# Kernel tuning notes

Hardware: AMD Instinct MI355X
Metric: run time of the kernel (lower is better)

The kernel has to match this reference:

```python
import jax, jax.numpy as jnp
import numpy as np

N = 100000       # nodes
E = 3200000      # edges (avg degree 32)
IN = 64          # in_channels
HID = 32         # hidden_channels
HEADS = 2
OUT = 1
EPS = 1e-5       # LayerNorm eps
SLOPE = 0.2      # LeakyReLU negative slope (PyG default)


def setup_inputs() -> dict:
    key = jax.random.key(0)
    ks = jax.random.split(key, 18)
    def nrm(k, shape, scale=0.1):
        return jax.random.normal(k, shape, dtype=jnp.float32) * scale
    return {
        "x": jax.random.normal(ks[0], (N, IN), dtype=jnp.float32),
        "edge_index": jax.random.randint(ks[1], (2, E), 0, N, dtype=jnp.int64),
        # GATConv layer 1 (concat=True)
        "W1": nrm(ks[2], (IN, HEADS * HID)),
        "a_src1": nrm(ks[3], (HEADS, HID)),
        "a_dst1": nrm(ks[4], (HEADS, HID)),
        "b1": jnp.zeros((HEADS * HID,), jnp.float32),
        "ln1_g": jnp.ones((HEADS * HID,), jnp.float32),
        "ln1_b": jnp.zeros((HEADS * HID,), jnp.float32),
        # GATConv layer 2 (heads=1, concat=False)
        "W2": nrm(ks[5], (HEADS * HID, HID)),
        "a_src2": nrm(ks[6], (1, HID)),
        "a_dst2": nrm(ks[7], (1, HID)),
        "b2": jnp.zeros((HID,), jnp.float32),
        "ln2_g": jnp.ones((HID,), jnp.float32),
        "ln2_b": jnp.zeros((HID,), jnp.float32),
        # output Linear
        "Wout": nrm(ks[8], (HID, OUT)),
        "bout": jnp.zeros((OUT,), jnp.float32),
    }


def layer_norm(x, g, b):
    mu = jnp.mean(x, axis=-1, keepdims=True)
    var = jnp.mean(jnp.square(x - mu), axis=-1, keepdims=True)
    return (x - mu) * jax.lax.rsqrt(var + EPS) * g + b


def gat_conv(x, edge_index, W, a_src, a_dst, bias, heads, ch, concat):
    """PyG GATConv (add_self_loops=True, bias=True), eval mode (no dropout)."""
    n = x.shape[0]
    loop = jnp.arange(n, dtype=edge_index.dtype)
    src = jnp.concatenate([edge_index[0], loop])   # [E+N]
    dst = jnp.concatenate([edge_index[1], loop])   # [E+N]
    h = (x @ W).reshape(n, heads, ch)              # [N,H,C]
    al_src = jnp.sum(h * a_src, axis=-1)           # [N,H]
    al_dst = jnp.sum(h * a_dst, axis=-1)           # [N,H]
    logits = jax.nn.leaky_relu(al_src[src] + al_dst[dst], SLOPE)  # [E+N,H]
    # segment softmax over destination nodes
    m = jax.lax.stop_gradient(jax.ops.segment_max(logits, dst, num_segments=n))
    e = jnp.exp(logits - m[dst])
    denom = jax.ops.segment_sum(e, dst, num_segments=n)
    alpha = e / denom[dst]                         # [E+N,H]
    out = jax.ops.segment_sum(h[src] * alpha[:, :, None], dst, num_segments=n)  # [N,H,C]
    out = out.reshape(n, heads * ch) if concat else out.mean(axis=1)
    return out + bias


def reference(x, edge_index, W1, a_src1, a_dst1, b1, ln1_g, ln1_b,
              W2, a_src2, a_dst2, b2, ln2_g, ln2_b, Wout, bout):
    h = gat_conv(x, edge_index, W1, a_src1, a_dst1, b1, HEADS, HID, True)
    h = jax.nn.elu(layer_norm(h, ln1_g, ln1_b))
    h = gat_conv(h, edge_index, W2, a_src2, a_dst2, b2, 1, HID, False)
    h = jax.nn.elu(layer_norm(h, ln2_g, ln2_b))
    return h @ Wout + bout  # [N, OUT]
```

## Files before the change

### kernel.cpp

```cpp
#include <hip/hip_runtime.h>

#define EPS 1e-5f
#define SLOPE 0.2f
#define MAXK 512
#define SEGCAP 12288
#define PBATCH 8192
#define AG1_SLOTS 8

__device__ __forceinline__ float leaky(float z) {
    return fmaxf(z, 0.f) + SLOPE * fminf(z, 0.f);
}
__device__ __forceinline__ ushort f2bf(float f) {
    unsigned u = __float_as_uint(f);
    u += 0x7FFFu + ((u >> 16) & 1u);
    return (ushort)(u >> 16);
}
__device__ __forceinline__ float bf2f(ushort b) {
    return __uint_as_float(((unsigned)b) << 16);
}
__device__ __forceinline__ float blo(unsigned u) {
    return __uint_as_float(u << 16);
}
__device__ __forceinline__ float bhi(unsigned u) {
    return __uint_as_float(u & 0xffff0000u);
}
__device__ __forceinline__ void gather16_to_lds(const void* g, void* l) {
    __builtin_amdgcn_global_load_lds(
        (const __attribute__((address_space(1))) void*)g,
        (__attribute__((address_space(3))) void*)l, 16, 0, 0);
}

__global__ __launch_bounds__(1024) void fused1(
    const int* __restrict__ ei, int E, int K, int* __restrict__ segcnt,
    unsigned* __restrict__ part,
    const float* __restrict__ x, const float* __restrict__ W1,
    const float* __restrict__ as1, const float* __restrict__ ad1,
    ushort* __restrict__ h1b, float* __restrict__ al_s, float* __restrict__ al_d,
    int N, int EB) {
    __shared__ float smem[4096 + 64 * 68];
    int t = threadIdx.x;
    if ((int)blockIdx.x < EB) {
        int* h   = (int*)smem;
        int* gp  = h + 512;
        int* run = h + 1024;
        for (int i = t; i < K; i += 1024) { h[i] = 0; run[i] = 0; }
        __syncthreads();
        int base = blockIdx.x * PBATCH;
        int sv[PBATCH / 1024], dv[PBATCH / 1024];
#pragma unroll
        for (int j = 0; j < PBATCH / 1024; j++) {
            int e = base + j * 1024 + t;
            sv[j] = (e < E) ? ei[e] : -1;
            dv[j] = (e < E) ? ei[E + e] : -1;
            if (dv[j] >= 0) atomicAdd(&h[dv[j] >> 8], 1);
        }
        __syncthreads();
        for (int i = t; i < K; i += 1024)
            gp[i] = h[i] ? atomicAdd(&segcnt[i * 16], h[i]) : 0;
        __syncthreads();
#pragma unroll
        for (int j = 0; j < PBATCH / 1024; j++) {
            if (dv[j] >= 0) {
                int b = dv[j] >> 8;
                int p = atomicAdd(&run[b], 1) + gp[b];
                if (p < SEGCAP)
                    part[(size_t)b * SEGCAP + p] =
                        ((unsigned)sv[j] << 8) | (unsigned)(dv[j] & 255);
            }
        }
        return;
    }
    float* Ws = smem;
    float (*xs)[68] = (float(*)[68])(smem + 4096);
    for (int i = t; i < 4096; i += 1024) Ws[i] = W1[i];
    int base = (blockIdx.x - EB) * 64;
    {
        int rr = t >> 4, kk = t & 15;
        int gr = base + rr;
        float4 vx = (gr < N) ? ((const float4*)x)[(size_t)gr * 16 + kk]
                             : make_float4(0.f, 0.f, 0.f, 0.f);
        *(float4*)&xs[rr][kk * 4] = vx;
    }
    __syncthreads();
    int wv = t >> 6, c = t & 63;
    int r0 = base + wv * 4;
    float acc0 = 0.f, acc1 = 0.f, acc2 = 0.f, acc3 = 0.f;
#pragma unroll
    for (int k = 0; k < 64; k += 4) {
        float4 x0 = *(const float4*)&xs[wv * 4 + 0][k];
        float4 x1 = *(const float4*)&xs[wv * 4 + 1][k];
        float4 x2 = *(const float4*)&xs[wv * 4 + 2][k];
        float4 x3 = *(const float4*)&xs[wv * 4 + 3][k];
        float w0 = Ws[(k + 0) * 64 + c];
        float w1 = Ws[(k + 1) * 64 + c];
        float w2 = Ws[(k + 2) * 64 + c];
        float w3 = Ws[(k + 3) * 64 + c];
        acc0 = fmaf(x0.x, w0, acc0); acc1 = fmaf(x1.x, w0, acc1);
        acc2 = fmaf(x2.x, w0, acc2); acc3 = fmaf(x3.x, w0, acc3);
        acc0 = fmaf(x0.y, w1, acc0); acc1 = fmaf(x1.y, w1, acc1);
        acc2 = fmaf(x2.y, w1, acc2); acc3 = fmaf(x3.y, w1, acc3);
        acc0 = fmaf(x0.z, w2, acc0); acc1 = fmaf(x1.z, w2, acc1);
        acc2 = fmaf(x2.z, w2, acc2); acc3 = fmaf(x3.z, w2, acc3);
        acc0 = fmaf(x0.w, w3, acc0); acc1 = fmaf(x1.w, w3, acc1);
        acc2 = fmaf(x2.w, w3, acc2); acc3 = fmaf(x3.w, w3, acc3);
    }
    int head = c >> 5, cc = c & 31;
    float asc = as1[head * 32 + cc], adc = ad1[head * 32 + cc];
    float vs0 = acc0 * asc, vd0 = acc0 * adc;
    float vs1 = acc1 * asc, vd1 = acc1 * adc;
    float vs2 = acc2 * asc, vd2 = acc2 * adc;
    float vs3 = acc3 * asc, vd3 = acc3 * adc;
#pragma unroll
    for (int off = 1; off < 32; off <<= 1) {
        vs0 += __shfl_xor(vs0, off); vd0 += __shfl_xor(vd0, off);
        vs1 += __shfl_xor(vs1, off); vd1 += __shfl_xor(vd1, off);
        vs2 += __shfl_xor(vs2, off); vd2 += __shfl_xor(vd2, off);
        vs3 += __shfl_xor(vs3, off); vd3 += __shfl_xor(vd3, off);
    }
    if (r0 + 0 < N) h1b[(size_t)(r0 + 0) * 64 + c] = f2bf(acc0);
    if (r0 + 1 < N) h1b[(size_t)(r0 + 1) * 64 + c] = f2bf(acc1);
    if (r0 + 2 < N) h1b[(size_t)(r0 + 2) * 64 + c] = f2bf(acc2);
    if (r0 + 3 < N) h1b[(size_t)(r0 + 3) * 64 + c] = f2bf(acc3);
    if (cc == 0) {
        if (r0 + 0 < N) { al_s[(r0 + 0) * 2 + head] = vs0; al_d[(r0 + 0) * 2 + head] = vd0; }
        if (r0 + 1 < N) { al_s[(r0 + 1) * 2 + head] = vs1; al_d[(r0 + 1) * 2 + head] = vd1; }
        if (r0 + 2 < N) { al_s[(r0 + 2) * 2 + head] = vs2; al_d[(r0 + 2) * 2 + head] = vd2; }
        if (r0 + 3 < N) { al_s[(r0 + 3) * 2 + head] = vs3; al_d[(r0 + 3) * 2 + head] = vd3; }
    }
}

__global__ __launch_bounds__(1024) void sortseg(
    const int* __restrict__ segcnt, int N,
    unsigned* __restrict__ part, int* __restrict__ nodeofs, int* __restrict__ cnt,
    int* __restrict__ perm) {
    __shared__ int h2[4096];
    __shared__ int ex[256];
    __shared__ int wsum[4];
    __shared__ unsigned outb[SEGCAP];
    int b = blockIdx.x, t = threadIdx.x;
    int lane = t & 63;
    size_t base = (size_t)b * SEGCAP;
    int sz = min(segcnt[b * 16], SEGCAP);
    for (int i = t; i < 4096; i += 1024) h2[i] = 0;
    __syncthreads();
    for (int i = t; i < sz; i += 1024) {
        unsigned code = part[base + i];
        int key = ((code & 255) << 4) | ((code >> 21) & 15);
        atomicAdd(&h2[key], 1);
    }
    __syncthreads();
    int v = 0;
    if (t < 256) {
#pragma unroll
        for (int i = 0; i < 16; i++) v += h2[t * 16 + i];
    }
    int incl = v;
#pragma unroll
    for (int off = 1; off < 64; off <<= 1) {
        int y = __shfl_up(incl, off);
        if (lane >= off) incl += y;
    }
    if (t < 256 && lane == 63) wsum[t >> 6] = incl;
    __syncthreads();
    if (t < 256) {
        int w = t >> 6;
        int wpre = 0;
#pragma unroll
        for (int k = 0; k < 4; k++) if (k < w) wpre += wsum[k];
        int exv = incl + wpre - v;
        int run = exv;
#pragma unroll
        for (int i = 0; i < 16; i++) {
            int lc = h2[t * 16 + i];
            h2[t * 16 + i] = run;
            run += lc;
        }
        int n = b * 256 + t;
        if (n < N) { cnt[n] = v; nodeofs[n] = (int)(base + exv); }
    }
    __syncthreads();
    for (int i = t; i < sz; i += 1024) {
        unsigned code = part[base + i];
        int key = ((code & 255) << 4) | ((code >> 21) & 15);
        int p = atomicAdd(&h2[key], 1);
        outb[p] = code >> 8;
    }
    __syncthreads();
    for (int i = t; i < sz; i += 1024) part[base + i] = outb[i];
    __syncthreads();
    if (t < 256) h2[t] = 0;
    __syncthreads();
    int n = b * 256 + t;
    int dbin = min(v, 255);
    if (t < 256 && n < N) atomicAdd(&h2[dbin], 1);
    __syncthreads();
    int hv = (t < 256) ? h2[t] : 0;
    int incl2 = hv;
#pragma unroll
    for (int off = 1; off < 64; off <<= 1) {
        int y = __shfl_up(incl2, off);
        if (lane >= off) incl2 += y;
    }
    if (t < 256 && lane == 63) wsum[t >> 6] = incl2;
    __syncthreads();
    if (t < 256) {
        int w = t >> 6;
        int wpre = 0;
#pragma unroll
        for (int k = 0; k < 4; k++) if (k < w) wpre += wsum[k];
        ex[t] = incl2 + wpre - hv;
    }
    __syncthreads();
    if (t < 256 && n < N) {
        int r = atomicAdd(&ex[dbin], 1);
        perm[b * 256 + r] = n;
    }
}

__global__ __launch_bounds__(256) void aggB1(
    const ushort* __restrict__ h1b, const float* __restrict__ als,
    const float* __restrict__ ald, const int* __restrict__ nodeofs,
    const int* __restrict__ cnt, const unsigned* __restrict__ csr,
    const int* __restrict__ perm,
    const float* __restrict__ b1, const float* __restrict__ g1,
    const float* __restrict__ bb1,
    const float* __restrict__ W2, const float* __restrict__ as2,
    const float* __restrict__ ad2, ushort* __restrict__ h2b,
    float* __restrict__ al2s, float* __restrict__ al2d, int N) {
    __shared__ uint4 stage[4][AG1_SLOTS * 64];
    __shared__ float W2s[64 * 32];
    int t = threadIdx.x;
    for (int i = t; i < 2048; i += 256) W2s[i] = W2[i];
    __syncthreads();
    int wid = t >> 6, lane = t & 63;
    int grp = lane >> 3, q = lane & 7;
    int gbase = grp << 3;
    uint4* mystage = stage[wid];
    int idx = blockIdx.x * 32 + wid * 8 + grp;
    bool valid = idx < N;
    int nc = perm[min(idx, N - 1)];
    int head = q >> 2;
    const float2* als2 = (const float2*)als;
    const float2* ald2 = (const float2*)ald;
    float2 adv = ald2[nc], asv = als2[nc];
    float ad0 = adv.x, ad1v = adv.y;
    float wsf = __expf(leaky((head ? asv.y : asv.x) + (head ? ad1v : ad0)));
    const uint4* h4 = (const uint4*)h1b;
    uint4 hs = h4[(size_t)nc * 8 + q];
    float a0 = wsf * blo(hs.x), a1 = wsf * bhi(hs.x);
    float a2 = wsf * blo(hs.y), a3 = wsf * bhi(hs.y);
    float a4 = wsf * blo(hs.z), a5 = wsf * bhi(hs.z);
    float a6 = wsf * blo(hs.w), a7 = wsf * bhi(hs.w);
    float lp0 = 0.f, lp1 = 0.f;
    int ofs = valid ? nodeofs[nc] : 0;
    int deg = valid ? cnt[nc] : 0;
    int degm1 = max(deg - 1, 0);
    int degmax = deg;
    degmax = max(degmax, __shfl_xor(degmax, 8));
    degmax = max(degmax, __shfl_xor(degmax, 16));
    degmax = max(degmax, __shfl_xor(degmax, 32));
    int sq = 0;
    if (degmax > 0) sq = min((int)csr[ofs + min(q, degm1)], N - 1);
    for (int eb = 0; eb < degmax; eb += AG1_SLOTS) {
#pragma unroll
        for (int k = 0; k < AG1_SLOTS; k++) {
            int s = __shfl(sq, gbase + k);
            gather16_to_lds(h4 + ((size_t)s * 8 + q), &mystage[k * 64]);
        }
        float2 av = als2[sq];
        int nsq = sq;
        int ebn = eb + AG1_SLOTS;
        if (ebn < degmax)
            nsq = min((int)csr[ofs + min(ebn + q, degm1)], N - 1);
        bool ev = (eb + q < deg);
        float w0 = ev ? __expf(leaky(av.x + ad0)) : 0.f;
        float w1 = ev ? __expf(leaky(av.y + ad1v)) : 0.f;
        lp0 += w0;
        lp1 += w1;
        asm volatile("s_waitcnt vmcnt(0)" ::: "memory");
        __builtin_amdgcn_sched_barrier(0);
#pragma unroll
        for (int k = 0; k < AG1_SLOTS; k++) {
            float wk0 = __shfl(w0, gbase + k);
            float wk1 = __shfl(w1, gbase + k);
            float w = head ? wk1 : wk0;
            uint4 hv = mystage[k * 64 + lane];
            a0 = fmaf(w, blo(hv.x), a0); a1 = fmaf(w, bhi(hv.x), a1);
            a2 = fmaf(w, blo(hv.y), a2); a3 = fmaf(w, bhi(hv.y), a3);
            a4 = fmaf(w, blo(hv.z), a4); a5 = fmaf(w, bhi(hv.z), a5);
            a6 = fmaf(w, blo(hv.w), a6); a7 = fmaf(w, bhi(hv.w), a7);
        }
        sq = nsq;
    }
#pragma unroll
    for (int off = 1; off < 8; off <<= 1) {
        lp0 += __shfl_xor(lp0, off);
        lp1 += __shfl_xor(lp1, off);
    }
    if (!valid) return;
    float l = (head ? lp1 : lp0) + wsf;
    float inv = 1.f / l;
    float4 bA = ((const float4*)b1)[2 * q];
    float4 bB = ((const float4*)b1)[2 * q + 1];
    float v0 = a0 * inv + bA.x, v1 = a1 * inv + bA.y;
    float v2 = a2 * inv + bA.z, v3 = a3 * inv + bA.w;
    float v4 = a4 * inv + bB.x, v5 = a5 * inv + bB.y;
    float v6 = a6 * inv + bB.z, v7 = a7 * inv + bB.w;
    float s1 = v0 + v1 + v2 + v3 + v4 + v5 + v6 + v7;
#pragma unroll
    for (int off = 1; off < 8; off <<= 1) s1 += __shfl_xor(s1, off);
    float mu = s1 * (1.f / 64.f);
    float d0 = v0 - mu, d1 = v1 - mu, d2 = v2 - mu, d3 = v3 - mu;
    float d4 = v4 - mu, d5 = v5 - mu, d6 = v6 - mu, d7 = v7 - mu;
    float s2v = d0 * d0 + d1 * d1 + d2 * d2 + d3 * d3
              + d4 * d4 + d5 * d5 + d6 * d6 + d7 * d7;
#pragma unroll
    for (int off = 1; off < 8; off <<= 1) s2v += __shfl_xor(s2v, off);
    float rs = rsqrtf(s2v * (1.f / 64.f) + EPS);
    float4 gA = ((const float4*)g1)[2 * q];
    float4 gB = ((const float4*)g1)[2 * q + 1];
    float4 cA = ((const float4*)bb1)[2 * q];
    float4 cB = ((const float4*)bb1)[2 * q + 1];
    float ya[8];
    ya[0] = d0 * rs * gA.x + cA.x;
    ya[1] = d1 * rs * gA.y + cA.y;
    ya[2] = d2 * rs * gA.z + cA.z;
    ya[3] = d3 * rs * gA.w + cA.w;
    ya[4] = d4 * rs * gB.x + cB.x;
    ya[5] = d5 * rs * gB.y + cB.y;
    ya[6] = d6 * rs * gB.z + cB.z;
    ya[7] = d7 * rs * gB.w + cB.w;
#pragma unroll
    for (int j = 0; j < 8; j++)
        ya[j] = (ya[j] > 0.f) ? ya[j] : (__expf(ya[j]) - 1.f);
    float o0 = 0.f, o1 = 0.f, o2 = 0.f, o3 = 0.f;
#pragma unroll
    for (int src = 0; src < 8; src++) {
#pragma unroll
        for (int j = 0; j < 8; j++) {
            float yv = __shfl(ya[j], gbase + src);
            float4 wr = *(const float4*)&W2s[(src * 8 + j) * 32 + 4 * q];
            o0 = fmaf(yv, wr.x, o0);
            o1 = fmaf(yv, wr.y, o1);
            o2 = fmaf(yv, wr.z, o2);
            o3 = fmaf(yv, wr.w, o3);
        }
    }
    ((ushort4*)h2b)[(size_t)nc * 8 + q] =
        make_ushort4(f2bf(o0), f2bf(o1), f2bf(o2), f2bf(o3));
    float4 a2v = ((const float4*)as2)[q];
    float4 d2v = ((const float4*)ad2)[q];
    float ps = o0 * a2v.x + o1 * a2v.y + o2 * a2v.z + o3 * a2v.w;
    float pd = o0 * d2v.x + o1 * d2v.y + o2 * d2v.z + o3 * d2v.w;
    ps += __shfl_xor(ps, 1); ps += __shfl_xor(ps, 2); ps += __shfl_xor(ps, 4);
    pd += __shfl_xor(pd, 1); pd += __shfl_xor(pd, 2); pd += __shfl_xor(pd, 4);
    if (q == 0) { al2s[nc] = ps; al2d[nc] = pd; }
}

__global__ __launch_bounds__(256, 2) void aggB2(
    const ushort* __restrict__ h2b, const float* __restrict__ als,
    const float* __restrict__ ald, const int* __restrict__ nodeofs,
    const int* __restrict__ cnt, const unsigned* __restrict__ csr,
    const int* __restrict__ perm,
    const float* __restrict__ b2, const float* __restrict__ g2,
    const float* __restrict__ bb2, const float* __restrict__ Wout,
    const float* __restrict__ bout, float* __restrict__ out, int N) {
    int lane = threadIdx.x & 63;
    int grp = lane >> 3, q = lane & 7;
    int gbase = grp << 3;
    int idx = blockIdx.x * 32 + (threadIdx.x >> 6) * 8 + grp;
    bool valid = idx < N;
    int nc = perm[min(idx, N - 1)];
    float myad = ald[nc];
    float wsf = __expf(leaky(als[nc] + myad));
    const ushort4* h4 = (const ushort4*)h2b;
    ushort4 hs = h4[(unsigned)nc * 8 + q];
    float a0 = wsf * bf2f(hs.x), a1 = wsf * bf2f(hs.y);
    float a2 = wsf * bf2f(hs.z), a3 = wsf * bf2f(hs.w);
    float lp = 0.f;
    int ofs = valid ? nodeofs[nc] : 0;
    int deg = valid ? cnt[nc] : 0;
    int degm1 = max(deg - 1, 0);
    int degmax = deg;
    degmax = max(degmax, __shfl_xor(degmax, 8));
    degmax = max(degmax, __shfl_xor(degmax, 16));
    degmax = max(degmax, __shfl_xor(degmax, 32));
    int sq0 = 0, sq1 = 0;
    if (degmax > 0) {
        int j0 = ofs + min(q, degm1);
        int j1 = ofs + min(8 + q, degm1);
        sq0 = min((int)csr[j0], N - 1);
        sq1 = min((int)csr[j1], N - 1);
    }
    for (int eb = 0; eb < degmax; eb += 16) {
        int s0[8], s1[8];
#pragma unroll
        for (int jj = 0; jj < 8; jj++) {
            s0[jj] = __shfl(sq0, gbase + jj);
            s1[jj] = __shfl(sq1, gbase + jj);
        }
        float av0 = als[sq0];
        float av1 = als[sq1];
        int nsq0 = sq0, nsq1 = sq1;
        int ebn = eb + 16;
        if (ebn < degmax) {
            int j0 = ofs + min(ebn + q, degm1);
            int j1 = ofs + min(ebn + 8 + q, degm1);
            nsq0 = min((int)csr[j0], N - 1);
            nsq1 = min((int)csr[j1], N - 1);
        }
        ushort4 r0[8], r1[8];
#pragma unroll
        for (int jj = 0; jj < 8; jj++) {
            r0[jj] = h4[(unsigned)s0[jj] * 8 + q];
            r1[jj] = h4[(unsigned)s1[jj] * 8 + q];
        }
        float z0 = leaky(av0 + myad);
        float z1 = leaky(av1 + myad);
        float wq0 = (eb + q < deg) ? __expf(z0) : 0.f;
        float wq1 = (eb + 8 + q < deg) ? __expf(z1) : 0.f;
        lp += wq0 + wq1;
        float w0a[8], w1a[8];
#pragma unroll
        for (int jj = 0; jj < 8; jj++) {
            w0a[jj] = __shfl(wq0, gbase + jj);
            w1a[jj] = __shfl(wq1, gbase + jj);
        }
#pragma unroll
        for (int jj = 0; jj < 8; jj++) {
            float w0 = w0a[jj], w1 = w1a[jj];
            a0 = fmaf(w0, bf2f(r0[jj].x), a0);
            a1 = fmaf(w0, bf2f(r0[jj].y), a1);
            a2 = fmaf(w0, bf2f(r0[jj].z), a2);
            a3 = fmaf(w0, bf2f(r0[jj].w), a3);
            a0 = fmaf(w1, bf2f(r1[jj].x), a0);
            a1 = fmaf(w1, bf2f(r1[jj].y), a1);
            a2 = fmaf(w1, bf2f(r1[jj].z), a2);
            a3 = fmaf(w1, bf2f(r1[jj].w), a3);
        }
        sq0 = nsq0;
        sq1 = nsq1;
    }
#pragma unroll
    for (int off = 1; off < 8; off <<= 1) lp += __shfl_xor(lp, off);
    if (!valid) return;
    float l = lp + wsf;
    float inv = 1.f / l;
    float4 bv = ((const float4*)b2)[q];
    float v0 = a0 * inv + bv.x, v1 = a1 * inv + bv.y;
    float v2 = a2 * inv + bv.z, v3 = a3 * inv + bv.w;
    float s1 = v0 + v1 + v2 + v3;
#pragma unroll
    for (int off = 1; off < 8; off <<= 1) s1 += __shfl_xor(s1, off);
    float mu = s1 * (1.f / 32.f);
    float d0 = v0 - mu, d1 = v1 - mu, d2 = v2 - mu, d3 = v3 - mu;
    float s2v = d0 * d0 + d1 * d1 + d2 * d2 + d3 * d3;
#pragma unroll
    for (int off = 1; off < 8; off <<= 1) s2v += __shfl_xor(s2v, off);
    float rs = rsqrtf(s2v * (1.f / 32.f) + EPS);
    float4 gv = ((const float4*)g2)[q];
    float4 bbv = ((const float4*)bb2)[q];
    float y0 = d0 * rs * gv.x + bbv.x;
    float y1 = d1 * rs * gv.y + bbv.y;
    float y2 = d2 * rs * gv.z + bbv.z;
    float y3 = d3 * rs * gv.w + bbv.w;
    y0 = (y0 > 0.f) ? y0 : (__expf(y0) - 1.f);
    y1 = (y1 > 0.f) ? y1 : (__expf(y1) - 1.f);
    y2 = (y2 > 0.f) ? y2 : (__expf(y2) - 1.f);
    y3 = (y3 > 0.f) ? y3 : (__expf(y3) - 1.f);
    float4 wo = ((const float4*)Wout)[q];
    float p = y0 * wo.x + y1 * wo.y + y2 * wo.z + y3 * wo.w;
#pragma unroll
    for (int off = 1; off < 8; off <<= 1) p += __shfl_xor(p, off);
    if (q == 0) out[nc] = p + bout[0];
}

extern "C" void kernel_launch(void* const* d_in, const int* in_sizes, int n_in,
                              void* d_out, int out_size, void* d_ws, size_t ws_size,
                              hipStream_t stream) {
    const float* x    = (const float*)d_in[0];
    const int*   ei   = (const int*)d_in[1];
    const float* W1   = (const float*)d_in[2];
    const float* as1  = (const float*)d_in[3];
    const float* ad1  = (const float*)d_in[4];
    const float* b1   = (const float*)d_in[5];
    const float* g1   = (const float*)d_in[6];
    const float* bb1  = (const float*)d_in[7];
    const float* W2   = (const float*)d_in[8];
    const float* as2  = (const float*)d_in[9];
    const float* ad2  = (const float*)d_in[10];
    const float* b2   = (const float*)d_in[11];
    const float* g2   = (const float*)d_in[12];
    const float* bb2  = (const float*)d_in[13];
    const float* Wout = (const float*)d_in[14];
    const float* bout = (const float*)d_in[15];
    float* out = (float*)d_out;

    const int N = in_sizes[0] / 64;
    const int E = in_sizes[1] / 2;
    const int K = (N + 255) / 256;

    auto align_up = [](size_t v) { return (v + 255) & ~(size_t)255; };
    char* ws = (char*)d_ws;
    unsigned* part    = (unsigned*)ws; ws += align_up((size_t)K * SEGCAP * 4);
    int*      segcnt  = (int*)ws;      ws += align_up((size_t)MAXK * 16 * 4);
    int*      nodeofs = (int*)ws;      ws += align_up((size_t)N * 4);
    int*      cnt     = (int*)ws;      ws += align_up((size_t)N * 4);
    int*      perm    = (int*)ws;      ws += align_up((size_t)(K * 256) * 4);
    ushort*   h1b     = (ushort*)ws;   ws += align_up((size_t)N * 64 * 2);
    ushort*   h2b     = (ushort*)ws;   ws += align_up((size_t)N * 32 * 2);
    float*    al1s    = (float*)ws;    ws += align_up((size_t)N * 2 * 4);
    float*    al1d    = (float*)ws;    ws += align_up((size_t)N * 2 * 4);
    float*    al2s    = (float*)ws;    ws += align_up((size_t)N * 4);
    float*    al2d    = (float*)ws;    ws += align_up((size_t)N * 4);

    const int EB = (E + PBATCH - 1) / PBATCH;
    const int PB = (N + 63) / 64;

    hipMemsetAsync(segcnt, 0, (size_t)K * 16 * 4, stream);
    fused1<<<EB + PB, 1024, 0, stream>>>(ei, E, K, segcnt, part,
                                         x, W1, as1, ad1, h1b, al1s, al1d, N, EB);
    sortseg<<<K, 1024, 0, stream>>>(segcnt, N, part, nodeofs, cnt, perm);
    aggB1<<<(N + 31) / 32, 256, 0, stream>>>(h1b, al1s, al1d, nodeofs, cnt, part,
                                             perm, b1, g1, bb1,
                                             W2, as2, ad2, h2b, al2s, al2d, N);
    aggB2<<<(N + 31) / 32, 256, 0, stream>>>(h2b, al2s, al2d, nodeofs, cnt, part,
                                             perm, b2, g2, bb2, Wout, bout, out, N);
}
```

Measured before the change: 298.2 us.

## Restructure layer-2 aggregation to 4 lanes per node with direct-to-LDS gathers

Rewrites aggB2 so each node is handled by 4 lanes, each owning 8 channels through 16-byte loads, instead of 8 lanes with 8-byte loads. Neighbor rows are fetched with a gather16_to_lds helper into per-wave shared staging slots (8 edges per iteration) and then read back from LDS for the weighted accumulation. Each block now covers 64 nodes, and the grid size is changed to match. The intent is wider memory transactions and fewer registers holding in-flight gathers. In exchange it adds LDS round-trips, a full vmcnt wait per batch, and half as many edges in flight per iteration.

```diff
diff --git a/kernel.cpp b/kernel.cpp
--- a/kernel.cpp
+++ b/kernel.cpp
@@ -6,6 +6,7 @@
 #define SEGCAP 12288
 #define PBATCH 8192
 #define AG1_SLOTS 8
+#define AG2_SLOTS 8
 
 __device__ __forceinline__ float leaky(float z) {
     return fmaxf(z, 0.f) + SLOPE * fminf(z, 0.f);
@@ -357,7 +358,7 @@
     if (q == 0) { al2s[nc] = ps; al2d[nc] = pd; }
 }
 
-__global__ __launch_bounds__(256, 2) void aggB2(
+__global__ __launch_bounds__(256) void aggB2(
     const ushort* __restrict__ h2b, const float* __restrict__ als,
     const float* __restrict__ ald, const int* __restrict__ nodeofs,
     const int* __restrict__ cnt, const unsigned* __restrict__ csr,
@@ -365,113 +366,115 @@
     const float* __restrict__ b2, const float* __restrict__ g2,
     const float* __restrict__ bb2, const float* __restrict__ Wout,
     const float* __restrict__ bout, float* __restrict__ out, int N) {
-    int lane = threadIdx.x & 63;
-    int grp = lane >> 3, q = lane & 7;
-    int gbase = grp << 3;
-    int idx = blockIdx.x * 32 + (threadIdx.x >> 6) * 8 + grp;
+    __shared__ uint4 stage[4][AG2_SLOTS * 64];
+    int t = threadIdx.x;
+    int wid = t >> 6, lane = t & 63;
+    int grp = lane >> 2, q = lane & 3;
+    int gbase = grp << 2;
+    uint4* mystage = stage[wid];
+    int idx = blockIdx.x * 64 + wid * 16 + grp;
     bool valid = idx < N;
     int nc = perm[min(idx, N - 1)];
     float myad = ald[nc];
     float wsf = __expf(leaky(als[nc] + myad));
-    const ushort4* h4 = (const ushort4*)h2b;
-    ushort4 hs = h4[(unsigned)nc * 8 + q];
-    float a0 = wsf * bf2f(hs.x), a1 = wsf * bf2f(hs.y);
-    float a2 = wsf * bf2f(hs.z), a3 = wsf * bf2f(hs.w);
+    const uint4* h4 = (const uint4*)h2b;
+    uint4 hs = h4[(size_t)nc * 4 + q];
+    float a0 = wsf * blo(hs.x), a1 = wsf * bhi(hs.x);
+    float a2 = wsf * blo(hs.y), a3 = wsf * bhi(hs.y);
+    float a4 = wsf * blo(hs.z), a5 = wsf * bhi(hs.z);
+    float a6 = wsf * blo(hs.w), a7 = wsf * bhi(hs.w);
     float lp = 0.f;
     int ofs = valid ? nodeofs[nc] : 0;
     int deg = valid ? cnt[nc] : 0;
     int degm1 = max(deg - 1, 0);
     int degmax = deg;
+    degmax = max(degmax, __shfl_xor(degmax, 4));
     degmax = max(degmax, __shfl_xor(degmax, 8));
     degmax = max(degmax, __shfl_xor(degmax, 16));
     degmax = max(degmax, __shfl_xor(degmax, 32));
     int sq0 = 0, sq1 = 0;
     if (degmax > 0) {
-        int j0 = ofs + min(q, degm1);
-        int j1 = ofs + min(8 + q, degm1);
-        sq0 = min((int)csr[j0], N - 1);
-        sq1 = min((int)csr[j1], N - 1);
-    }
-    for (int eb = 0; eb < degmax; eb += 16) {
-        int s0[8], s1[8];
-#pragma unroll
-        for (int jj = 0; jj < 8; jj++) {
-            s0[jj] = __shfl(sq0, gbase + jj);
-            s1[jj] = __shfl(sq1, gbase + jj);
+        sq0 = min((int)csr[ofs + min(q, degm1)], N - 1);
+        sq1 = min((int)csr[ofs + min(4 + q, degm1)], N - 1);
+    }
+    for (int eb = 0; eb < degmax; eb += AG2_SLOTS) {
+#pragma unroll
+        for (int k = 0; k < AG2_SLOTS; k++) {
+            int s = (k < 4) ? __shfl(sq0, gbase + k)
+                            : __shfl(sq1, gbase + (k - 4));
+            gather16_to_lds(h4 + ((size_t)s * 4 + q), &mystage[k * 64]);
         }
         float av0 = als[sq0];
         float av1 = als[sq1];
         int nsq0 = sq0, nsq1 = sq1;
-        int ebn = eb + 16;
+        int ebn = eb + AG2_SLOTS;
         if (ebn < degmax) {
-            int j0 = ofs + min(ebn + q, degm1);
-            int j1 = ofs + min(ebn + 8 + q, degm1);
-            nsq0 = min((int)csr[j0], N - 1);
-            nsq1 = min((int)csr[j1], N - 1);
-        }
-        ushort4 r0[8], r1[8];
-#pragma unroll
-        for (int jj = 0; jj < 8; jj++) {
-            r0[jj] = h4[(unsigned)s0[jj] * 8 + q];
-            r1[jj] = h4[(unsigned)s1[jj] * 8 + q];
-        }
-        float z0 = leaky(av0 + myad);
-        float z1 = leaky(av1 + myad);
-        float wq0 = (eb + q < deg) ? __expf(z0) : 0.f;
-        float wq1 = (eb + 8 + q < deg) ? __expf(z1) : 0.f;
+            nsq0 = min((int)csr[ofs + min(ebn + q, degm1)], N - 1);
+            nsq1 = min((int)csr[ofs + min(ebn + 4 + q, degm1)], N - 1);
+        }
+        float wq0 = (eb + q < deg) ? __expf(leaky(av0 + myad)) : 0.f;
+        float wq1 = (eb + 4 + q < deg) ? __expf(leaky(av1 + myad)) : 0.f;
         lp += wq0 + wq1;
-        float w0a[8], w1a[8];
-#pragma unroll
-        for (int jj = 0; jj < 8; jj++) {
-            w0a[jj] = __shfl(wq0, gbase + jj);
-            w1a[jj] = __shfl(wq1, gbase + jj);
-        }
-#pragma unroll
-        for (int jj = 0; jj < 8; jj++) {
-            float w0 = w0a[jj], w1 = w1a[jj];
-            a0 = fmaf(w0, bf2f(r0[jj].x), a0);
-            a1 = fmaf(w0, bf2f(r0[jj].y), a1);
-            a2 = fmaf(w0, bf2f(r0[jj].z), a2);
-            a3 = fmaf(w0, bf2f(r0[jj].w), a3);
-            a0 = fmaf(w1, bf2f(r1[jj].x), a0);
-            a1 = fmaf(w1, bf2f(r1[jj].y), a1);
-            a2 = fmaf(w1, bf2f(r1[jj].z), a2);
-            a3 = fmaf(w1, bf2f(r1[jj].w), a3);
+        asm volatile("s_waitcnt vmcnt(0)" ::: "memory");
+        __builtin_amdgcn_sched_barrier(0);
+#pragma unroll
+        for (int k = 0; k < AG2_SLOTS; k++) {
+            float w = (k < 4) ? __shfl(wq0, gbase + k)
+                              : __shfl(wq1, gbase + (k - 4));
+            uint4 hv = mystage[k * 64 + lane];
+            a0 = fmaf(w, blo(hv.x), a0); a1 = fmaf(w, bhi(hv.x), a1);
+            a2 = fmaf(w, blo(hv.y), a2); a3 = fmaf(w, bhi(hv.y), a3);
+            a4 = fmaf(w, blo(hv.z), a4); a5 = fmaf(w, bhi(hv.z), a5);
+            a6 = fmaf(w, blo(hv.w), a6); a7 = fmaf(w, bhi(hv.w), a7);
         }
         sq0 = nsq0;
         sq1 = nsq1;
     }
-#pragma unroll
-    for (int off = 1; off < 8; off <<= 1) lp += __shfl_xor(lp, off);
+    lp += __shfl_xor(lp, 1);
+    lp += __shfl_xor(lp, 2);
     if (!valid) return;
     float l = lp + wsf;
     float inv = 1.f / l;
-    float4 bv = ((const float4*)b2)[q];
-    float v0 = a0 * inv + bv.x, v1 = a1 * inv + bv.y;
-    float v2 = a2 * inv + bv.z, v3 = a3 * inv + bv.w;
-    float s1 = v0 + v1 + v2 + v3;
-#pragma unroll
-    for (int off = 1; off < 8; off <<= 1) s1 += __shfl_xor(s1, off);
+    float4 bA = ((const float4*)b2)[2 * q];
+    float4 bB = ((const float4*)b2)[2 * q + 1];
+    float v0 = a0 * inv + bA.x, v1 = a1 * inv + bA.y;
+    float v2 = a2 * inv + bA.z, v3 = a3 * inv + bA.w;
+    float v4 = a4 * inv + bB.x, v5 = a5 * inv + bB.y;
+    float v6 = a6 * inv + bB.z, v7 = a7 * inv + bB.w;
+    float s1 = v0 + v1 + v2 + v3 + v4 + v5 + v6 + v7;
+    s1 += __shfl_xor(s1, 1); s1 += __shfl_xor(s1, 2);
     float mu = s1 * (1.f / 32.f);
     float d0 = v0 - mu, d1 = v1 - mu, d2 = v2 - mu, d3 = v3 - mu;
-    float s2v = d0 * d0 + d1 * d1 + d2 * d2 + d3 * d3;
-#pragma unroll
-    for (int off = 1; off < 8; off <<= 1) s2v += __shfl_xor(s2v, off);
+    float d4 = v4 - mu, d5 = v5 - mu, d6 = v6 - mu, d7 = v7 - mu;
+    float s2v = d0 * d0 + d1 * d1 + d2 * d2 + d3 * d3
+              + d4 * d4 + d5 * d5 + d6 * d6 + d7 * d7;
+    s2v += __shfl_xor(s2v, 1); s2v += __shfl_xor(s2v, 2);
     float rs = rsqrtf(s2v * (1.f / 32.f) + EPS);
-    float4 gv = ((const float4*)g2)[q];
-    float4 bbv = ((const float4*)bb2)[q];
-    float y0 = d0 * rs * gv.x + bbv.x;
-    float y1 = d1 * rs * gv.y + bbv.y;
-    float y2 = d2 * rs * gv.z + bbv.z;
-    float y3 = d3 * rs * gv.w + bbv.w;
+    float4 gA = ((const float4*)g2)[2 * q];
+    float4 gB = ((const float4*)g2)[2 * q + 1];
+    float4 cA = ((const float4*)bb2)[2 * q];
+    float4 cB = ((const float4*)bb2)[2 * q + 1];
+    float y0 = d0 * rs * gA.x + cA.x;
+    float y1 = d1 * rs * gA.y + cA.y;
+    float y2 = d2 * rs * gA.z + cA.z;
+    float y3 = d3 * rs * gA.w + cA.w;
+    float y4 = d4 * rs * gB.x + cB.x;
+    float y5 = d5 * rs * gB.y + cB.y;
+    float y6 = d6 * rs * gB.z + cB.z;
+    float y7 = d7 * rs * gB.w + cB.w;
     y0 = (y0 > 0.f) ? y0 : (__expf(y0) - 1.f);
     y1 = (y1 > 0.f) ? y1 : (__expf(y1) - 1.f);
     y2 = (y2 > 0.f) ? y2 : (__expf(y2) - 1.f);
     y3 = (y3 > 0.f) ? y3 : (__expf(y3) - 1.f);
-    float4 wo = ((const float4*)Wout)[q];
-    float p = y0 * wo.x + y1 * wo.y + y2 * wo.z + y3 * wo.w;
-#pragma unroll
-    for (int off = 1; off < 8; off <<= 1) p += __shfl_xor(p, off);
+    y4 = (y4 > 0.f) ? y4 : (__expf(y4) - 1.f);
+    y5 = (y5 > 0.f) ? y5 : (__expf(y5) - 1.f);
+    y6 = (y6 > 0.f) ? y6 : (__expf(y6) - 1.f);
+    y7 = (y7 > 0.f) ? y7 : (__expf(y7) - 1.f);
+    float4 wA = ((const float4*)Wout)[2 * q];
+    float4 wB = ((const float4*)Wout)[2 * q + 1];
+    float p = y0 * wA.x + y1 * wA.y + y2 * wA.z + y3 * wA.w
+            + y4 * wB.x + y5 * wB.y + y6 * wB.z + y7 * wB.w;
+    p += __shfl_xor(p, 1); p += __shfl_xor(p, 2);
     if (q == 0) out[nc] = p + bout[0];
 }
 
@@ -524,6 +527,6 @@
     aggB1<<<(N + 31) / 32, 256, 0, stream>>>(h1b, al1s, al1d, nodeofs, cnt, part,
                                              perm, b1, g1, bb1,
                                              W2, as2, ad2, h2b, al2s, al2d, N);
-    aggB2<<<(N + 31) / 32, 256, 0, stream>>>(h2b, al2s, al2d, nodeofs, cnt, part,
+    aggB2<<<(N + 63) / 64, 256, 0, stream>>>(h2b, al2s, al2d, nodeofs, cnt, part,
                                              perm, b2, g2, bb2, Wout, bout, out, N);
 }
```

Result: no change. 300.7 us (+0.9%).
